# Performance work log

Hardware: AMD Instinct MI355X
Metric: run time of the kernel (lower is better)

## Reference

```python
import jax, jax.numpy as jnp
import numpy as np

B, H, W, C = 4, 64, 64, 32
M1 = M2 = 16
N = H * W          # 4096 grid nodes per sample
E = 131072         # edges (avg degree 32)
EDIM = 6           # edge feature dim
KMID = 64          # kernel MLP hidden width
EPS = 1e-5         # InstanceNorm eps


def _gelu(x):
    return jax.nn.gelu(x, approximate=False)  # torch nn.GELU default is exact erf


def _mlp(x, w1, b1, w2, b2):
    return _gelu(x @ w1 + b1) @ w2 + b2


def _inorm(x):
    # torch InstanceNorm2d(affine=False) applied to [B,H,W,C]: normalizes over last two dims
    m = x.mean(axis=(2, 3), keepdims=True)
    v = x.var(axis=(2, 3), keepdims=True)
    return (x - m) * jax.lax.rsqrt(v + EPS)


def _lin_init(k, fin, fout):
    lim = 1.0 / np.sqrt(fin)
    kw, kb = jax.random.split(k)
    w = jax.random.uniform(kw, (fin, fout), jnp.float32, -lim, lim)
    b = jax.random.uniform(kb, (fout,), jnp.float32, -lim, lim)
    return w, b


def setup_inputs() -> dict:
    key = jax.random.key(0)
    ks = jax.random.split(key, 14)
    s = 1.0 / (C * C)
    inp = {}
    inp['nodes'] = jax.random.normal(ks[0], (B, H, W, C), jnp.float32)
    inp['edge_index'] = jax.random.randint(ks[1], (2, E), 0, N, dtype=jnp.int64)
    inp['edge_attr'] = jax.random.uniform(ks[2], (E, EDIM), jnp.float32)
    # spectral conv complex weights, stored as real/imag float32 pairs
    inp['w1_re'] = s * jax.random.uniform(ks[3], (C, C, M1, M2), jnp.float32)
    inp['w1_im'] = s * jax.random.uniform(ks[4], (C, C, M1, M2), jnp.float32)
    inp['w2_re'] = s * jax.random.uniform(ks[5], (C, C, M1, M2), jnp.float32)
    inp['w2_im'] = s * jax.random.uniform(ks[6], (C, C, M1, M2), jnp.float32)
    # self.mlp : MLP(C, C, 2C)
    inp['mlp_w1'], inp['mlp_b1'] = _lin_init(ks[7], C, 2 * C)
    inp['mlp_w2'], inp['mlp_b2'] = _lin_init(ks[8], 2 * C, C)
    # self.w : MLP(C, C, 2C)
    inp['wm_w1'], inp['wm_b1'] = _lin_init(ks[9], C, 2 * C)
    inp['wm_w2'], inp['wm_b2'] = _lin_init(ks[10], 2 * C, C)
    # GNO kernel MLP : EDIM -> KMID -> C*C
    inp['ker_w1'], inp['ker_b1'] = _lin_init(ks[11], EDIM, KMID)
    inp['ker_w2'], inp['ker_b2'] = _lin_init(ks[12], KMID, C * C)
    # NNConv root weight and bias (PyG uniform(size) init with size=in_channels)
    lim = 1.0 / np.sqrt(C)
    kr, kb = jax.random.split(ks[13])
    inp['root'] = jax.random.uniform(kr, (C, C), jnp.float32, -lim, lim)
    inp['gbias'] = jax.random.uniform(kb, (C,), jnp.float32, -lim, lim)
    return inp


def reference(nodes, edge_index, edge_attr, w1_re, w1_im, w2_re, w2_im,
              mlp_w1, mlp_b1, mlp_w2, mlp_b2, wm_w1, wm_b1, wm_w2, wm_b2,
              ker_w1, ker_b1, ker_w2, ker_b2, root, gbias):
    x = _inorm(nodes)                                             # [B,H,W,C]

    # --- spectral conv branch ---
    x_ft = jnp.fft.rfftn(x, axes=(1, 2), norm='ortho')            # [B,H,W//2+1,C]
    w1 = (w1_re + 1j * w1_im).astype(jnp.complex64)
    w2 = (w2_re + 1j * w2_im).astype(jnp.complex64)
    top = jnp.einsum('bxyi,ioxy->bxyo', x_ft[:, :M1, :M2, :], w1)
    bot = jnp.einsum('bxyi,ioxy->bxyo', x_ft[:, -M1:, :M2, :], w2)
    out_ft = jnp.zeros((B, H, W // 2 + 1, C), jnp.complex64)
    out_ft = out_ft.at[:, :M1, :M2, :].set(top).at[:, -M1:, :M2, :].set(bot)
    x1 = jnp.fft.irfftn(out_ft, axes=(1, 2), s=(H, W), norm='ortho')
    x1 = _mlp(_inorm(x1), mlp_w1, mlp_b1, mlp_w2, mlp_b2)         # [B,H,W,C]

    # --- pointwise MLP branch ---
    x2 = _inorm(_mlp(x, wm_w1, wm_b1, wm_w2, wm_b2))              # [B,H,W,C]

    # --- edge-conditioned GNO branch ---
    x3 = x.reshape(B, N, C)
    wmat = _mlp(edge_attr, ker_w1, ker_b1, ker_w2, ker_b2).reshape(E, C, C)
    src, dst = edge_index[0], edge_index[1]
    msg = jnp.einsum('bec,eco->beo', x3[:, src, :], wmat)         # [B,E,C]
    agg = jnp.zeros((B, N, C), jnp.float32).at[:, dst, :].add(msg)
    x3 = agg + x3 @ root + gbias                                  # [B,N,C]

    return _gelu(x1 + x2 + x3.reshape(B, H, W, C))
```

## Files before the change

### kernel.cpp

```cpp
#include <hip/hip_runtime.h>

#define E_ 131072

typedef _Float16 half8 __attribute__((ext_vector_type(8)));
typedef float f32x4 __attribute__((ext_vector_type(4)));

__device__ __forceinline__ float gelu_f(float x) {
    return 0.5f * x * (1.0f + erff(x * 0.70710678118654752f));
}

#define TWOPI_64 (6.2831853071795864769f / 64.0f)

__device__ __forceinline__ void block_reduce2(float& s, float& s2, float* red) {
    #pragma unroll
    for (int off = 32; off > 0; off >>= 1) {
        s  += __shfl_down(s, off, 64);
        s2 += __shfl_down(s2, off, 64);
    }
    int lane = threadIdx.x & 63, wv = threadIdx.x >> 6;
    __syncthreads();
    if (lane == 0) { red[wv] = s; red[wv + 4] = s2; }
    __syncthreads();
    s  = red[0] + red[1] + red[2] + red[3];
    s2 = red[4] + red[5] + red[6] + red[7];
}

__device__ __forceinline__ void gno_body(int e0, float* sbufF, float* sB2, int* ssrc, int* sdst,
                                         const float* __restrict__ ea,
                                         const float* __restrict__ kw1, const float* __restrict__ kb1,
                                         const float* __restrict__ kb2,
                                         const _Float16* __restrict__ whi, const _Float16* __restrict__ wlo,
                                         const float* __restrict__ xn, const int* __restrict__ ei,
                                         float* __restrict__ agg) {
    _Float16* sxTh = (_Float16*)sbufF;
    int t = threadIdx.x;
    int lane = t & 63, wv = t >> 6, quad = lane >> 4, l15 = lane & 15;
    int eg = wv >> 1, t2 = wv & 1;

    if (t < 64) ssrc[t] = ei[e0 + t];
    else if (t < 128) sdst[t - 64] = ei[E_ + e0 + t - 64];
    for (int f = t; f < 1024; f += 256) sB2[f] = kb2[f];
    {
        int r = t >> 2, k0 = (t & 3) * 16;
        const float* ep = ea + (e0 + r) * 6;
        float e6[6];
        #pragma unroll
        for (int d = 0; d < 6; ++d) e6[d] = ep[d];
        #pragma unroll
        for (int kk = 0; kk < 16; ++kk) {
            int k = k0 + kk;
            float acc = kb1[k];
            #pragma unroll
            for (int d = 0; d < 6; ++d) acc += e6[d] * kw1[d * 64 + k];
            sbufF[r * 68 + k] = gelu_f(acc);
        }
    }
    __syncthreads();
    half8 ahi[2][2], alo[2][2];
    #pragma unroll
    for (int et = 0; et < 2; ++et) {
        #pragma unroll
        for (int kh = 0; kh < 2; ++kh) {
            const float* hp = sbufF + (eg * 32 + et * 16 + l15) * 68 + kh * 32 + quad * 8;
            float4 h0 = *(const float4*)hp;
            float4 h1 = *(const float4*)(hp + 4);
            float hv[8] = {h0.x, h0.y, h0.z, h0.w, h1.x, h1.y, h1.z, h1.w};
            half8 hh, hl;
            #pragma unroll
            for (int j = 0; j < 8; ++j) {
                _Float16 hi = (_Float16)hv[j];
                hh[j] = hi;
                hl[j] = (_Float16)(hv[j] - (float)hi);
            }
            ahi[et][kh] = hh;
            alo[et][kh] = hl;
        }
    }
    __syncthreads();
    {
        int b = t & 3, r = t >> 2;
        int s = ssrc[r];
        int pe = (r >> 5) * 32 + ((r >> 2) & 3) * 8 + ((r >> 4) & 1) * 4 + (r & 3);
        const float4* xp = (const float4*)(xn + (b * 4096 + s) * 32);
        _Float16* dp = sxTh + b * 2312 + pe;
        #pragma unroll
        for (int q = 0; q < 8; ++q) {
            float4 v = xp[q];
            dp[(q * 4 + 0) * 72] = (_Float16)v.x;
            dp[(q * 4 + 1) * 72] = (_Float16)v.y;
            dp[(q * 4 + 2) * 72] = (_Float16)v.z;
            dp[(q * 4 + 3) * 72] = (_Float16)v.w;
        }
    }
    __syncthreads();
    float msg[4][2][4];
    #pragma unroll
    for (int b = 0; b < 4; ++b)
        #pragma unroll
        for (int et = 0; et < 2; ++et)
            #pragma unroll
            for (int r = 0; r < 4; ++r) msg[b][et][r] = 0.f;

    for (int i = 0; i < 32; ++i) {
        float b2v = sB2[i * 32 + t2 * 16 + l15];
        int f0 = (i * 4 + t2 * 2) * 512 + lane * 8;
        half8 bhi0 = *(const half8*)(whi + f0);
        half8 bhi1 = *(const half8*)(whi + f0 + 512);
        half8 blo0 = *(const half8*)(wlo + f0);
        half8 blo1 = *(const half8*)(wlo + f0 + 512);
        f32x4 acc[2];
        #pragma unroll
        for (int et = 0; et < 2; ++et) {
            f32x4 ac = {b2v, b2v, b2v, b2v};
            ac = __builtin_amdgcn_mfma_f32_16x16x32_f16(ahi[et][0], bhi0, ac, 0, 0, 0);
            ac = __builtin_amdgcn_mfma_f32_16x16x32_f16(ahi[et][1], bhi1, ac, 0, 0, 0);
            ac = __builtin_amdgcn_mfma_f32_16x16x32_f16(ahi[et][0], blo0, ac, 0, 0, 0);
            ac = __builtin_amdgcn_mfma_f32_16x16x32_f16(ahi[et][1], blo1, ac, 0, 0, 0);
            ac = __builtin_amdgcn_mfma_f32_16x16x32_f16(alo[et][0], bhi0, ac, 0, 0, 0);
            ac = __builtin_amdgcn_mfma_f32_16x16x32_f16(alo[et][1], bhi1, ac, 0, 0, 0);
            acc[et] = ac;
        }
        #pragma unroll
        for (int b = 0; b < 4; ++b) {
            const half8 xv = *(const half8*)(sxTh + b * 2312 + i * 72 + eg * 32 + quad * 8);
            #pragma unroll
            for (int et = 0; et < 2; ++et) {
                msg[b][et][0] += (float)xv[et * 4 + 0] * acc[et][0];
                msg[b][et][1] += (float)xv[et * 4 + 1] * acc[et][1];
                msg[b][et][2] += (float)xv[et * 4 + 2] * acc[et][2];
                msg[b][et][3] += (float)xv[et * 4 + 3] * acc[et][3];
            }
        }
    }
    int o = t2 * 16 + l15;
    #pragma unroll
    for (int et = 0; et < 2; ++et) {
        #pragma unroll
        for (int r = 0; r < 4; ++r) {
            int row = eg * 32 + et * 16 + quad * 4 + r;
            int d = sdst[row];
            #pragma unroll
            for (int b = 0; b < 4; ++b) {
                atomicAdd(&agg[(b * 4096 + d) * 32 + o], msg[b][et][r]);
            }
        }
    }
}

__global__ __launch_bounds__(256, 4) void k_pre(const float* __restrict__ nodes,
                                                const float* __restrict__ w2,
                                                const float* __restrict__ ww1, const float* __restrict__ wb1,
                                                const float* __restrict__ ww2, const float* __restrict__ wb2,
                                                float* __restrict__ xn,
                                                float* __restrict__ agg,
                                                float* __restrict__ osum,
                                                float* __restrict__ Gre, float* __restrict__ Gim,
                                                _Float16* __restrict__ whi, _Float16* __restrict__ wlo) {
    int t = threadIdx.x;
    if (blockIdx.x >= 256) {
        int g0 = (blockIdx.x - 256) * 512 + t;
        #pragma unroll 1
        for (int rep = 0; rep < 2; ++rep) {
            int g = g0 + rep * 256;
            int j = g & 7, l = (g >> 3) & 63, fid = g >> 9;
            int i = fid >> 2, t2 = (fid >> 1) & 1, kh = fid & 1;
            int quad = l >> 4, l15 = l & 15;
            int k = kh * 32 + quad * 8 + j;
            int n = i * 32 + t2 * 16 + l15;
            float v = w2[k * 1024 + n];
            _Float16 hi = (_Float16)v;
            whi[g] = hi;
            wlo[g] = (_Float16)(v - (float)hi);
        }
        return;
    }
    int bh = blockIdx.x;
    __shared__ float sx[2112];
    __shared__ float tc[64], ts[64];
    __shared__ float red[8];
    __shared__ float sW1[2048], sW2[2048];
    __shared__ float sH[4160];
    const float4* src = (const float4*)(nodes + bh * 2048);
    float4* dst = (float4*)(xn + bh * 2048);
    float4* az = (float4*)(agg + bh * 2048);
    if (t < 64) { float a = TWOPI_64 * t; tc[t] = cosf(a); ts[t] = sinf(a); }
    for (int f = t; f < 2048; f += 256) { sW1[f] = ww1[f]; sW2[f] = ww2[f]; }
    float4 v0 = src[t * 2], v1 = src[t * 2 + 1];
    float s  = v0.x + v0.y + v0.z + v0.w + v1.x + v1.y + v1.z + v1.w;
    float s2 = v0.x*v0.x + v0.y*v0.y + v0.z*v0.z + v0.w*v0.w
             + v1.x*v1.x + v1.y*v1.y + v1.z*v1.z + v1.w*v1.w;
    block_reduce2(s, s2, red);
    float mean = s * (1.0f / 2048.0f);
    float var  = s2 * (1.0f / 2048.0f) - mean * mean;
    float sc = rsqrtf(var + 1e-5f);
    v0.x = (v0.x - mean) * sc; v0.y = (v0.y - mean) * sc;
    v0.z = (v0.z - mean) * sc; v0.w = (v0.w - mean) * sc;
    v1.x = (v1.x - mean) * sc; v1.y = (v1.y - mean) * sc;
    v1.z = (v1.z - mean) * sc; v1.w = (v1.w - mean) * sc;
    dst[t * 2] = v0; dst[t * 2 + 1] = v1;
    float4 z = {0.f, 0.f, 0.f, 0.f};
    az[t * 2] = z; az[t * 2 + 1] = z;
    {
        int w = t >> 2, c0 = (t & 3) * 8;
        float* p = sx + w * 33 + c0;
        p[0] = v0.x; p[1] = v0.y; p[2] = v0.z; p[3] = v0.w;
        p[4] = v1.x; p[5] = v1.y; p[6] = v1.z; p[7] = v1.w;
    }
    __syncthreads();
    #pragma unroll 1
    for (int rep = 0; rep < 2; ++rep) {
        int oi = rep * 256 + t;
        int ky = oi >> 5, i = oi & 31;
        float re = 0.f, im = 0.f;
        #pragma unroll 8
        for (int w = 0; w < 64; ++w) {
            float v = sx[w * 33 + i];
            int m = (ky * w) & 63;
            re += v * tc[m];
            im -= v * ts[m];
        }
        Gre[bh * 512 + oi] = re;
        Gim[bh * 512 + oi] = im;
    }
    __syncthreads();
    #pragma unroll 1
    for (int rep = 0; rep < 16; ++rep) {
        int idx = rep * 256 + t;
        int w = idx >> 6, k = idx & 63;
        float acc = wb1[k];
        #pragma unroll 4
        for (int c = 0; c < 32; ++c) acc += sx[w * 33 + c] * sW1[c * 64 + k];
        sH[w * 65 + k] = gelu_f(acc);
    }
    __syncthreads();
    s = 0.f; s2 = 0.f;
    #pragma unroll 1
    for (int rep = 0; rep < 8; ++rep) {
        int idx = rep * 256 + t;
        int w = idx >> 5, o = idx & 31;
        float acc = wb2[o];
        #pragma unroll 4
        for (int k = 0; k < 64; ++k) acc += sH[w * 65 + k] * sW2[k * 32 + o];
        sW1[idx] = acc;
        s += acc; s2 += acc * acc;
    }
    block_reduce2(s, s2, red);
    mean = s * (1.0f / 2048.0f);
    sc = rsqrtf(s2 * (1.0f / 2048.0f) - mean * mean + 1e-5f);
    #pragma unroll 1
    for (int rep = 0; rep < 8; ++rep) {
        int idx = rep * 256 + t;
        osum[bh * 2048 + idx] = (sW1[idx] - mean) * sc;
    }
}

__global__ __launch_bounds__(256, 4) void k_g1(
        const float* __restrict__ Gre, const float* __restrict__ Gim,
        const float* __restrict__ w1re, const float* __restrict__ w1im,
        const float* __restrict__ w2re, const float* __restrict__ w2im,
        float* __restrict__ Yr, float* __restrict__ Yi,
        const float* __restrict__ ea,
        const float* __restrict__ kw1, const float* __restrict__ kb1,
        const float* __restrict__ kb2,
        const _Float16* __restrict__ whi, const _Float16* __restrict__ wlo,
        const float* __restrict__ xn,
        const int* __restrict__ ei,
        float* __restrict__ agg) {
    __shared__ __align__(16) float U[5648];
    __shared__ int ssrc[64], sdst[64];
    int t = threadIdx.x;

    if (blockIdx.x < 128) {
        float* tc  = U;
        float* ts  = U + 64;
        float* sXr = U + 128;
        float* sXi = U + 656;
        int bid = blockIdx.x;
        int b = bid >> 5, kxi = bid & 31;
        int kx = kxi + (kxi < 16 ? 0 : 32);
        int x = kxi & 15;
        const float* wre = (kxi < 16) ? w1re : w2re;
        const float* wim = (kxi < 16) ? w1im : w2im;
        if (t < 64) { float a = TWOPI_64 * t; tc[t] = cosf(a); ts[t] = sinf(a); }
        __syncthreads();
        #pragma unroll 1
        for (int rep = 0; rep < 2; ++rep) {
            int oi = rep * 256 + t;
            int ky = oi >> 5, i = oi & 31;
            float re = 0.f, im = 0.f;
            #pragma unroll 8
            for (int h = 0; h < 64; ++h) {
                int gidx = (b * 64 + h) * 512 + ky * 32 + i;
                float gr = Gre[gidx], gi = Gim[gidx];
                int m = (kx * h) & 63;
                float c = tc[m], sv = ts[m];
                re += gr * c + gi * sv;
                im += gi * c - gr * sv;
            }
            sXr[ky * 33 + i] = re;
            sXi[ky * 33 + i] = im;
        }
        __syncthreads();
        #pragma unroll 1
        for (int rep = 0; rep < 2; ++rep) {
            int oi = rep * 256 + t;
            int ky = oi & 15, o = oi >> 4;
            float re = 0.f, im = 0.f;
            #pragma unroll 4
            for (int i = 0; i < 32; ++i) {
                float xr = sXr[ky * 33 + i], xi = sXi[ky * 33 + i];
                int widx = (i * 32 + o) * 256 + x * 16 + ky;
                float wr = wre[widx], wi = wim[widx];
                re += xr * wr - xi * wi;
                im += xr * wi + xi * wr;
            }
            Yr[bid * 512 + ky * 32 + o] = re;
            Yi[bid * 512 + ky * 32 + o] = im;
        }
        return;
    }
    gno_body((blockIdx.x - 128) * 64, U, U + 4624, ssrc, sdst,
             ea, kw1, kb1, kb2, whi, wlo, xn, ei, agg);
}

__global__ __launch_bounds__(256, 4) void k_g2(
        const float* __restrict__ Yr, const float* __restrict__ Yi,
        const float* __restrict__ mw1, const float* __restrict__ mb1,
        const float* __restrict__ mw2, const float* __restrict__ mb2,
        float* __restrict__ osum,
        const float* __restrict__ ea,
        const float* __restrict__ kw1, const float* __restrict__ kb1,
        const float* __restrict__ kb2,
        const _Float16* __restrict__ whi, const _Float16* __restrict__ wlo,
        const float* __restrict__ xn,
        const int* __restrict__ ei,
        float* __restrict__ agg) {
    __shared__ __align__(16) float U[11584];
    __shared__ int ssrc[64], sdst[64];
    int t = threadIdx.x;

    if (blockIdx.x < 256) {
        int bh = blockIdx.x;
        int b = bh >> 6, h = bh & 63;
        float* tc  = U;
        float* ts  = U + 64;
        float* red = U + 128;
        float* sZr = U + 136;
        float* sZi = U + 664;
        float* sP  = U + 1192;
        float* sW1 = U + 3304;
        float* sW2 = U + 5352;
        float* sH  = U + 7400;
        if (t < 64) { float a = TWOPI_64 * t; tc[t] = cosf(a); ts[t] = sinf(a); }
        for (int f = t; f < 2048; f += 256) { sW1[f] = mw1[f]; sW2[f] = mw2[f]; }
        __syncthreads();
        #pragma unroll 1
        for (int rep = 0; rep < 2; ++rep) {
            int oi = rep * 256 + t;
            int ky = oi >> 5, o = oi & 31;
            float re = 0.f, im = 0.f;
            #pragma unroll 4
            for (int kxi = 0; kxi < 32; ++kxi) {
                int kx = kxi + (kxi < 16 ? 0 : 32);
                int m = (kx * h) & 63;
                float c = tc[m], sv = ts[m];
                int yidx = (b * 32 + kxi) * 512 + ky * 32 + o;
                float yr = Yr[yidx], yi = Yi[yidx];
                re += yr * c - yi * sv;
                im += yr * sv + yi * c;
            }
            sZr[ky * 33 + o] = re;
            sZi[ky * 33 + o] = im;
        }
        __syncthreads();
        float s = 0.f, s2 = 0.f;
        #pragma unroll 1
        for (int rep = 0; rep < 8; ++rep) {
            int idx = rep * 256 + t;
            int w = idx >> 5, o = idx & 31;
            float acc = sZr[o];
            #pragma unroll
            for (int ky = 1; ky < 16; ++ky) {
                int m = (ky * w) & 63;
                acc += 2.0f * (sZr[ky * 33 + o] * tc[m] - sZi[ky * 33 + o] * ts[m]);
            }
            acc *= (1.0f / 4096.0f);
            sP[w * 33 + o] = acc;
            s += acc; s2 += acc * acc;
        }
        block_reduce2(s, s2, red);
        float mean = s * (1.0f / 2048.0f);
        float sc = rsqrtf(s2 * (1.0f / 2048.0f) - mean * mean + 1e-5f);
        #pragma unroll 1
        for (int rep = 0; rep < 8; ++rep) {
            int idx = rep * 256 + t;
            int w = idx >> 5, o = idx & 31;
            sP[w * 33 + o] = (sP[w * 33 + o] - mean) * sc;
        }
        __syncthreads();
        #pragma unroll 1
        for (int rep = 0; rep < 16; ++rep) {
            int idx = rep * 256 + t;
            int w = idx >> 6, k = idx & 63;
            float acc = mb1[k];
            #pragma unroll 4
            for (int c = 0; c < 32; ++c) acc += sP[w * 33 + c] * sW1[c * 64 + k];
            sH[w * 65 + k] = gelu_f(acc);
        }
        __syncthreads();
        #pragma unroll 1
        for (int rep = 0; rep < 8; ++rep) {
            int idx = rep * 256 + t;
            int w = idx >> 5, o = idx & 31;
            float acc = mb2[o];
            #pragma unroll 4
            for (int k = 0; k < 64; ++k) acc += sH[w * 65 + k] * sW2[k * 32 + o];
            osum[bh * 2048 + idx] += acc;
        }
        return;
    }
    gno_body((1152 + blockIdx.x - 256) * 64, U, U + 4624, ssrc, sdst,
             ea, kw1, kb1, kb2, whi, wlo, xn, ei, agg);
}

__global__ __launch_bounds__(256, 4) void k_final(const float* __restrict__ osum, const float* __restrict__ agg,
                                                  const float* __restrict__ xn, const float* __restrict__ root,
                                                  const float* __restrict__ gbias, float* __restrict__ out) {
    int bh = blockIdx.x >> 2, q = blockIdx.x & 3;
    int base = bh * 2048 + q * 512;
    int t = threadIdx.x;
    __shared__ float sX[16 * 33];
    __shared__ float sR[1024];
    for (int f = t; f < 512; f += 256) sX[(f >> 5) * 33 + (f & 31)] = xn[base + f];
    for (int f = t; f < 1024; f += 256) sR[f] = root[f];
    __syncthreads();
    #pragma unroll 1
    for (int rep = 0; rep < 2; ++rep) {
        int idx = rep * 256 + t;
        int w = idx >> 5, o = idx & 31;
        float acc = gbias[o] + osum[base + idx] + agg[base + idx];
        #pragma unroll 4
        for (int c = 0; c < 32; ++c) acc += sX[w * 33 + c] * sR[c * 32 + o];
        out[base + idx] = gelu_f(acc);
    }
}

extern "C" void kernel_launch(void* const* d_in, const int* in_sizes, int n_in,
                              void* d_out, int out_size, void* d_ws, size_t ws_size,
                              hipStream_t stream) {
    (void)in_sizes; (void)n_in; (void)out_size; (void)ws_size;
    const float* nodes  = (const float*)d_in[0];
    const int*   eidx   = (const int*)d_in[1];
    const float* eattr  = (const float*)d_in[2];
    const float* w1re   = (const float*)d_in[3];
    const float* w1im   = (const float*)d_in[4];
    const float* w2re   = (const float*)d_in[5];
    const float* w2im   = (const float*)d_in[6];
    const float* mlp_w1 = (const float*)d_in[7];
    const float* mlp_b1 = (const float*)d_in[8];
    const float* mlp_w2 = (const float*)d_in[9];
    const float* mlp_b2 = (const float*)d_in[10];
    const float* wm_w1  = (const float*)d_in[11];
    const float* wm_b1  = (const float*)d_in[12];
    const float* wm_w2  = (const float*)d_in[13];
    const float* wm_b2  = (const float*)d_in[14];
    const float* ker_w1 = (const float*)d_in[15];
    const float* ker_b1 = (const float*)d_in[16];
    const float* ker_w2 = (const float*)d_in[17];
    const float* ker_b2 = (const float*)d_in[18];
    const float* root   = (const float*)d_in[19];
    const float* gbias  = (const float*)d_in[20];
    float* out = (float*)d_out;

    char* ws = (char*)d_ws;
    size_t off = 0;
    auto alloc = [&](size_t bytes) {
        void* p = ws + off;
        off += (bytes + 255) & ~(size_t)255;
        return p;
    };
    float* xn   = (float*)alloc(524288 * 4);
    float* agg  = (float*)alloc(524288 * 4);
    float* osum = (float*)alloc(524288 * 4);
    float* Gre  = (float*)alloc(131072 * 4);
    float* Gim  = (float*)alloc(131072 * 4);
    float* Yr   = (float*)alloc(65536 * 4);
    float* Yi   = (float*)alloc(65536 * 4);
    _Float16* whi = (_Float16*)alloc(65536 * 2);
    _Float16* wlo = (_Float16*)alloc(65536 * 2);

    k_pre<<<384, 256, 0, stream>>>(nodes, ker_w2, wm_w1, wm_b1, wm_w2, wm_b2,
                                   xn, agg, osum, Gre, Gim, whi, wlo);
    k_g1<<<1280, 256, 0, stream>>>(Gre, Gim, w1re, w1im, w2re, w2im, Yr, Yi,
                                   eattr, ker_w1, ker_b1, ker_b2, whi, wlo, xn, eidx, agg);
    k_g2<<<1152, 256, 0, stream>>>(Yr, Yi, mlp_w1, mlp_b1, mlp_w2, mlp_b2, osum,
                                   eattr, ker_w1, ker_b1, ker_b2, whi, wlo, xn, eidx, agg);
    k_final<<<1024, 256, 0, stream>>>(osum, agg, xn, root, gbias, out);
}
```

Measured before the change: 254.4 us.

## Move pointwise MLP branch into k_g1 and shrink shared memory via fp16 hidden

Takes the pointwise MLP plus instance-norm branch out of k_pre and runs it as 256 extra blocks inside k_g1, alongside the spectral and GNO blocks. The MLP weights are now read straight from global/L1 instead of being staged in shared memory, and the hidden activations are kept in LDS as fp16. This cuts the LDS footprint of k_pre and k_g2 to allow more resident blocks and balances work across kernels, and the GNO edge ranges are rebalanced between k_g1 and k_g2. In exchange the hidden layer loses precision through fp16 rounding, and the weight loads are repeated from cache.

```diff
diff --git a/kernel.cpp b/kernel.cpp
--- a/kernel.cpp
+++ b/kernel.cpp
@@ -149,11 +149,8 @@
 
 __global__ __launch_bounds__(256, 4) void k_pre(const float* __restrict__ nodes,
                                                 const float* __restrict__ w2,
-                                                const float* __restrict__ ww1, const float* __restrict__ wb1,
-                                                const float* __restrict__ ww2, const float* __restrict__ wb2,
                                                 float* __restrict__ xn,
                                                 float* __restrict__ agg,
-                                                float* __restrict__ osum,
                                                 float* __restrict__ Gre, float* __restrict__ Gim,
                                                 _Float16* __restrict__ whi, _Float16* __restrict__ wlo) {
     int t = threadIdx.x;
@@ -175,16 +172,13 @@
         return;
     }
     int bh = blockIdx.x;
-    __shared__ float sx[2112];
+    __shared__ float sx[2048];
     __shared__ float tc[64], ts[64];
     __shared__ float red[8];
-    __shared__ float sW1[2048], sW2[2048];
-    __shared__ float sH[4160];
     const float4* src = (const float4*)(nodes + bh * 2048);
     float4* dst = (float4*)(xn + bh * 2048);
     float4* az = (float4*)(agg + bh * 2048);
     if (t < 64) { float a = TWOPI_64 * t; tc[t] = cosf(a); ts[t] = sinf(a); }
-    for (int f = t; f < 2048; f += 256) { sW1[f] = ww1[f]; sW2[f] = ww2[f]; }
     float4 v0 = src[t * 2], v1 = src[t * 2 + 1];
     float s  = v0.x + v0.y + v0.z + v0.w + v1.x + v1.y + v1.z + v1.w;
     float s2 = v0.x*v0.x + v0.y*v0.y + v0.z*v0.z + v0.w*v0.w
@@ -200,12 +194,8 @@
     dst[t * 2] = v0; dst[t * 2 + 1] = v1;
     float4 z = {0.f, 0.f, 0.f, 0.f};
     az[t * 2] = z; az[t * 2 + 1] = z;
-    {
-        int w = t >> 2, c0 = (t & 3) * 8;
-        float* p = sx + w * 33 + c0;
-        p[0] = v0.x; p[1] = v0.y; p[2] = v0.z; p[3] = v0.w;
-        p[4] = v1.x; p[5] = v1.y; p[6] = v1.z; p[7] = v1.w;
-    }
+    ((float4*)sx)[t * 2] = v0;
+    ((float4*)sx)[t * 2 + 1] = v1;
     __syncthreads();
     #pragma unroll 1
     for (int rep = 0; rep < 2; ++rep) {
@@ -214,43 +204,13 @@
         float re = 0.f, im = 0.f;
         #pragma unroll 8
         for (int w = 0; w < 64; ++w) {
-            float v = sx[w * 33 + i];
+            float v = sx[w * 32 + i];
             int m = (ky * w) & 63;
             re += v * tc[m];
             im -= v * ts[m];
         }
         Gre[bh * 512 + oi] = re;
         Gim[bh * 512 + oi] = im;
-    }
-    __syncthreads();
-    #pragma unroll 1
-    for (int rep = 0; rep < 16; ++rep) {
-        int idx = rep * 256 + t;
-        int w = idx >> 6, k = idx & 63;
-        float acc = wb1[k];
-        #pragma unroll 4
-        for (int c = 0; c < 32; ++c) acc += sx[w * 33 + c] * sW1[c * 64 + k];
-        sH[w * 65 + k] = gelu_f(acc);
-    }
-    __syncthreads();
-    s = 0.f; s2 = 0.f;
-    #pragma unroll 1
-    for (int rep = 0; rep < 8; ++rep) {
-        int idx = rep * 256 + t;
-        int w = idx >> 5, o = idx & 31;
-        float acc = wb2[o];
-        #pragma unroll 4
-        for (int k = 0; k < 64; ++k) acc += sH[w * 65 + k] * sW2[k * 32 + o];
-        sW1[idx] = acc;
-        s += acc; s2 += acc * acc;
-    }
-    block_reduce2(s, s2, red);
-    mean = s * (1.0f / 2048.0f);
-    sc = rsqrtf(s2 * (1.0f / 2048.0f) - mean * mean + 1e-5f);
-    #pragma unroll 1
-    for (int rep = 0; rep < 8; ++rep) {
-        int idx = rep * 256 + t;
-        osum[bh * 2048 + idx] = (sW1[idx] - mean) * sc;
     }
 }
 
@@ -259,6 +219,9 @@
         const float* __restrict__ w1re, const float* __restrict__ w1im,
         const float* __restrict__ w2re, const float* __restrict__ w2im,
         float* __restrict__ Yr, float* __restrict__ Yi,
+        const float* __restrict__ ww1, const float* __restrict__ wb1,
+        const float* __restrict__ ww2, const float* __restrict__ wb2,
+        float* __restrict__ osum,
         const float* __restrict__ ea,
         const float* __restrict__ kw1, const float* __restrict__ kb1,
         const float* __restrict__ kb2,
@@ -319,7 +282,46 @@
         }
         return;
     }
-    gno_body((blockIdx.x - 128) * 64, U, U + 4624, ssrc, sdst,
+    if (blockIdx.x < 384) {
+        int bh = blockIdx.x - 128;
+        float* red = U;
+        float* sX = U + 8;
+        _Float16* sHh = (_Float16*)(U + 2120);
+        for (int f = t; f < 2048; f += 256) sX[(f >> 5) * 33 + (f & 31)] = xn[bh * 2048 + f];
+        __syncthreads();
+        #pragma unroll 1
+        for (int rep = 0; rep < 16; ++rep) {
+            int idx = rep * 256 + t;
+            int w = idx >> 6, k = idx & 63;
+            float acc = wb1[k];
+            #pragma unroll 4
+            for (int c = 0; c < 32; ++c) acc += sX[w * 33 + c] * ww1[c * 64 + k];
+            sHh[w * 72 + k] = (_Float16)gelu_f(acc);
+        }
+        __syncthreads();
+        float s = 0.f, s2 = 0.f;
+        #pragma unroll 1
+        for (int rep = 0; rep < 8; ++rep) {
+            int idx = rep * 256 + t;
+            int w = idx >> 5, o = idx & 31;
+            float acc = wb2[o];
+            #pragma unroll 4
+            for (int k = 0; k < 64; ++k) acc += (float)sHh[w * 72 + k] * ww2[k * 32 + o];
+            sX[w * 33 + o] = acc;
+            s += acc; s2 += acc * acc;
+        }
+        block_reduce2(s, s2, red);
+        float mean = s * (1.0f / 2048.0f);
+        float sc = rsqrtf(s2 * (1.0f / 2048.0f) - mean * mean + 1e-5f);
+        #pragma unroll 1
+        for (int rep = 0; rep < 8; ++rep) {
+            int idx = rep * 256 + t;
+            int w = idx >> 5, o = idx & 31;
+            osum[bh * 2048 + idx] = (sX[w * 33 + o] - mean) * sc;
+        }
+        return;
+    }
+    gno_body((blockIdx.x - 384) * 64, U, U + 4624, ssrc, sdst,
              ea, kw1, kb1, kb2, whi, wlo, xn, ei, agg);
 }
 
@@ -335,7 +337,7 @@
         const float* __restrict__ xn,
         const int* __restrict__ ei,
         float* __restrict__ agg) {
-    __shared__ __align__(16) float U[11584];
+    __shared__ __align__(16) float U[5648];
     __shared__ int ssrc[64], sdst[64];
     int t = threadIdx.x;
 
@@ -348,11 +350,8 @@
         float* sZr = U + 136;
         float* sZi = U + 664;
         float* sP  = U + 1192;
-        float* sW1 = U + 3304;
-        float* sW2 = U + 5352;
-        float* sH  = U + 7400;
+        _Float16* sHh = (_Float16*)(U + 3304);
         if (t < 64) { float a = TWOPI_64 * t; tc[t] = cosf(a); ts[t] = sinf(a); }
-        for (int f = t; f < 2048; f += 256) { sW1[f] = mw1[f]; sW2[f] = mw2[f]; }
         __syncthreads();
         #pragma unroll 1
         for (int rep = 0; rep < 2; ++rep) {
@@ -404,8 +403,8 @@
             int w = idx >> 6, k = idx & 63;
             float acc = mb1[k];
             #pragma unroll 4
-            for (int c = 0; c < 32; ++c) acc += sP[w * 33 + c] * sW1[c * 64 + k];
-            sH[w * 65 + k] = gelu_f(acc);
+            for (int c = 0; c < 32; ++c) acc += sP[w * 33 + c] * mw1[c * 64 + k];
+            sHh[w * 72 + k] = (_Float16)gelu_f(acc);
         }
         __syncthreads();
         #pragma unroll 1
@@ -414,12 +413,12 @@
             int w = idx >> 5, o = idx & 31;
             float acc = mb2[o];
             #pragma unroll 4
-            for (int k = 0; k < 64; ++k) acc += sH[w * 65 + k] * sW2[k * 32 + o];
+            for (int k = 0; k < 64; ++k) acc += (float)sHh[w * 72 + k] * mw2[k * 32 + o];
             osum[bh * 2048 + idx] += acc;
         }
         return;
     }
-    gno_body((1152 + blockIdx.x - 256) * 64, U, U + 4624, ssrc, sdst,
+    gno_body((1024 + blockIdx.x - 256) * 64, U, U + 4624, ssrc, sdst,
              ea, kw1, kb1, kb2, whi, wlo, xn, ei, agg);
 }
 
@@ -489,11 +488,11 @@
     _Float16* whi = (_Float16*)alloc(65536 * 2);
     _Float16* wlo = (_Float16*)alloc(65536 * 2);
 
-    k_pre<<<384, 256, 0, stream>>>(nodes, ker_w2, wm_w1, wm_b1, wm_w2, wm_b2,
-                                   xn, agg, osum, Gre, Gim, whi, wlo);
-    k_g1<<<1280, 256, 0, stream>>>(Gre, Gim, w1re, w1im, w2re, w2im, Yr, Yi,
+    k_pre<<<384, 256, 0, stream>>>(nodes, ker_w2, xn, agg, Gre, Gim, whi, wlo);
+    k_g1<<<1408, 256, 0, stream>>>(Gre, Gim, w1re, w1im, w2re, w2im, Yr, Yi,
+                                   wm_w1, wm_b1, wm_w2, wm_b2, osum,
                                    eattr, ker_w1, ker_b1, ker_b2, whi, wlo, xn, eidx, agg);
-    k_g2<<<1152, 256, 0, stream>>>(Yr, Yi, mlp_w1, mlp_b1, mlp_w2, mlp_b2, osum,
+    k_g2<<<1280, 256, 0, stream>>>(Yr, Yi, mlp_w1, mlp_b1, mlp_w2, mlp_b2, osum,
                                    eattr, ker_w1, ker_b1, ker_b2, whi, wlo, xn, eidx, agg);
     k_final<<<1024, 256, 0, stream>>>(osum, agg, xn, root, gbias, out);
 }
```

Measured after the change: 247.3 us. 1.03x faster.
